# Kernel tuning notes

Hardware: AMD Instinct MI355X
Metric: run time of the kernel (lower is better)

## Reference

```python
import jax, jax.numpy as jnp
import numpy as np

DIM = 1024
NUM_HEADS = 16
HEAD_DIM = DIM // NUM_HEADS
ROPE_BASE = 10000.0


def _rope_cache(seq_len, head_dim, dtype=jnp.float32):
    inv_freq = 1.0 / (ROPE_BASE ** (jnp.arange(0, head_dim, 2, dtype=jnp.float32) / head_dim))
    t = jnp.arange(seq_len, dtype=jnp.float32)
    freqs = jnp.einsum('i,j->ij', t, inv_freq)          # [S, hd/2]
    emb = jnp.concatenate([freqs, freqs], axis=-1)       # [S, hd]
    return jnp.cos(emb).astype(dtype), jnp.sin(emb).astype(dtype)


def _rotate_half(x):
    x1, x2 = jnp.split(x, 2, axis=-1)
    return jnp.concatenate([-x2, x1], axis=-1)


def setup_inputs() -> dict:
    key = jax.random.key(0)
    k1, k2, k3 = jax.random.split(key, 3)
    B, S, D = 2, 2048, DIM
    x = jax.random.normal(k1, (B, S, D), dtype=jnp.float32)
    mask = jnp.tril(jnp.ones((S, S), dtype=jnp.bool_))   # causal mask
    w_qkv = jax.random.normal(k2, (D, 3 * D), dtype=jnp.float32) * (D ** -0.5)
    w_out = jax.random.normal(k3, (D, D), dtype=jnp.float32) * (D ** -0.5)
    return {"x": x, "w_qkv": w_qkv, "w_out": w_out, "mask": mask}


def reference(x, w_qkv, w_out, mask):
    B, S, D = x.shape
    H, hd = NUM_HEADS, HEAD_DIM
    qkv = x @ w_qkv                                       # [B,S,3D]
    q, k, v = jnp.split(qkv, 3, axis=-1)
    # [B,H,S,hd]
    q = q.reshape(B, S, H, hd).transpose(0, 2, 1, 3)
    k = k.reshape(B, S, H, hd).transpose(0, 2, 1, 3)
    v = v.reshape(B, S, H, hd).transpose(0, 2, 1, 3)
    cos, sin = _rope_cache(S, hd, q.dtype)               # [S,hd]
    q = q * cos + _rotate_half(q) * sin
    k = k * cos + _rotate_half(k) * sin
    scale = hd ** -0.5
    scores = jnp.einsum('bhqd,bhkd->bhqk', q, k) * scale  # [B,H,S,S]
    neg = jnp.finfo(scores.dtype).min
    scores = jnp.where(mask[None, None, :, :], scores, neg)
    attn = jax.nn.softmax(scores, axis=-1)                # dropout off (eval)
    out = jnp.einsum('bhqk,bhkd->bhqd', attn, v)
    out = out.transpose(0, 2, 1, 3).reshape(B, S, D)
    return out @ w_out
```

## Files before the change

### kernel.cpp

```cpp
#include <hip/hip_runtime.h>

typedef __attribute__((ext_vector_type(8))) short short8;
typedef __attribute__((ext_vector_type(4))) float f32x4;
typedef __attribute__((ext_vector_type(16))) float f32x16;

__device__ __forceinline__ unsigned short f2bf(float f) {
    unsigned u = __builtin_bit_cast(unsigned, f);
    u += 0x7FFFu + ((u >> 16) & 1u);
    return (unsigned short)(u >> 16);
}
__device__ __forceinline__ float bf2f(unsigned short b) {
    unsigned u = ((unsigned)b) << 16;
    return __builtin_bit_cast(float, u);
}
__device__ __forceinline__ short8 ld_frag(const uint4* p, size_t idx16) {
    return __builtin_bit_cast(short8, p[idx16]);
}
__device__ __forceinline__ unsigned cvt_pk_bf16(float lo, float hi) {
    unsigned r;
    asm("v_cvt_pk_bf16_f32 %0, %1, %2" : "=v"(r) : "v"(lo), "v"(hi));
    return r;
}
__device__ __forceinline__ void gload_lds16(const void* g, void* l) {
    __builtin_amdgcn_global_load_lds((const __attribute__((address_space(1))) void*)g,
                                     (__attribute__((address_space(3))) void*)l, 16, 0, 0);
}

__global__ void rope_table_kernel(float* cosT, float* sinT) {
    int idx = blockIdx.x * 256 + threadIdx.x;
    int s = idx >> 5, i = idx & 31;
    float inv = powf(10000.f, -(float)i / 32.f);
    float ang = (float)s * inv;
    cosT[idx] = cosf(ang);
    sinT[idx] = sinf(ang);
}

__global__ void cast_x_kernel(const float* __restrict__ x, unsigned short* __restrict__ xb) {
    int i = blockIdx.x * 256 + threadIdx.x;
    float4 v = reinterpret_cast<const float4*>(x)[i];
    ushort4 o;
    o.x = f2bf(v.x); o.y = f2bf(v.y); o.z = f2bf(v.z); o.w = f2bf(v.w);
    reinterpret_cast<ushort4*>(xb)[i] = o;
}

__global__ void transpose_cast_kernel(const float* __restrict__ in, unsigned short* __restrict__ out,
                                      int R, int C) {
    __shared__ float t[32][33];
    int c0 = blockIdx.x * 32, r0 = blockIdx.y * 32;
    int tx = threadIdx.x, ty = threadIdx.y;
    for (int i = 0; i < 4; ++i)
        t[ty + i * 8][tx] = in[(size_t)(r0 + ty + i * 8) * C + c0 + tx];
    __syncthreads();
    for (int i = 0; i < 4; ++i)
        out[(size_t)(c0 + ty + i * 8) * R + r0 + tx] = f2bf(t[tx][ty + i * 8]);
}

template <bool OUT_BF16, int NF>
__global__ __launch_bounds__(256) void gemm_bt_kernel(const unsigned short* __restrict__ A,
                                                      const unsigned short* __restrict__ Bt,
                                                      void* __restrict__ Cout,
                                                      int M, int N, int K) {
    constexpr int BN = NF * 32;
    __shared__ __align__(16) unsigned short As[2][128 * 32];
    __shared__ __align__(16) unsigned short Bs[2][BN * 32];
    int tid = threadIdx.x;
    int lane = tid & 63;
    int w = tid >> 6;
    int wm = w >> 1, wn = w & 1;
    int m0 = blockIdx.y * 128, n0 = blockIdx.x * BN;
    int rq = lane >> 4, cl = lane & 15;

    f32x4 acc[4][NF] = {};
    const uint4* As4 = reinterpret_cast<const uint4*>(As);
    const uint4* Bs4 = reinterpret_cast<const uint4*>(Bs);

    #pragma unroll
    for (int i = 0; i < 2; ++i) {
        int c = i * 256 + tid;
        int r = c >> 2, cc = c & 3;
        gload_lds16(A + (size_t)(m0 + r) * K + cc * 8,
                    (char*)As[0] + (size_t)(i * 256 + w * 64) * 16);
    }
    #pragma unroll
    for (int i = 0; i < NF / 2; ++i) {
        int c = i * 256 + tid;
        int r = c >> 2, cc = c & 3;
        gload_lds16(Bt + (size_t)(n0 + r) * K + cc * 8,
                    (char*)Bs[0] + (size_t)(i * 256 + w * 64) * 16);
    }
    __syncthreads();
    int cur = 0;

    for (int k0 = 0; k0 < K; k0 += 32) {
        short8 af[4], bfr[NF];
        #pragma unroll
        for (int mf = 0; mf < 4; ++mf) {
            int row = wm * 64 + mf * 16 + cl;
            af[mf] = ld_frag(As4, cur * 512 + row * 4 + rq);
        }
        #pragma unroll
        for (int nf = 0; nf < NF; ++nf) {
            int row = wn * (NF * 16) + nf * 16 + cl;
            bfr[nf] = ld_frag(Bs4, cur * (NF * 128) + row * 4 + rq);
        }
        if (k0 + 32 < K) {
            int kn = k0 + 32;
            #pragma unroll
            for (int i = 0; i < 2; ++i) {
                int c = i * 256 + tid;
                int r = c >> 2, cc = c & 3;
                gload_lds16(A + (size_t)(m0 + r) * K + kn + cc * 8,
                            (char*)As[cur ^ 1] + (size_t)(i * 256 + w * 64) * 16);
            }
            #pragma unroll
            for (int i = 0; i < NF / 2; ++i) {
                int c = i * 256 + tid;
                int r = c >> 2, cc = c & 3;
                gload_lds16(Bt + (size_t)(n0 + r) * K + kn + cc * 8,
                            (char*)Bs[cur ^ 1] + (size_t)(i * 256 + w * 64) * 16);
            }
        }
        __builtin_amdgcn_s_setprio(1);
        #pragma unroll
        for (int mf = 0; mf < 4; ++mf)
            #pragma unroll
            for (int nf = 0; nf < NF; ++nf)
                acc[mf][nf] = __builtin_amdgcn_mfma_f32_16x16x32_bf16(af[mf], bfr[nf], acc[mf][nf], 0, 0, 0);
        __builtin_amdgcn_s_setprio(0);
        __syncthreads();
        cur ^= 1;
    }
    #pragma unroll
    for (int mf = 0; mf < 4; ++mf)
        #pragma unroll
        for (int nf = 0; nf < NF; ++nf)
            #pragma unroll
            for (int r = 0; r < 4; ++r) {
                size_t row = m0 + wm * 64 + mf * 16 + rq * 4 + r;
                size_t col = n0 + wn * (NF * 16) + nf * 16 + cl;
                float v = acc[mf][nf][r];
                if (OUT_BF16)
                    ((unsigned short*)Cout)[row * N + col] = f2bf(v);
                else
                    ((float*)Cout)[row * N + col] = v;
            }
}

__global__ __launch_bounds__(256) void gemm_qkv_rope_kernel(const unsigned short* __restrict__ A,
                                                            const unsigned short* __restrict__ Bt,
                                                            const float* __restrict__ cosT,
                                                            const float* __restrict__ sinT,
                                                            unsigned short* __restrict__ Qb,
                                                            unsigned short* __restrict__ Kb,
                                                            unsigned short* __restrict__ VT) {
    const int K = 1024;
    __shared__ __align__(16) unsigned short As[2][128 * 32];
    __shared__ __align__(16) unsigned short Bs[2][128 * 32];
    int tid = threadIdx.x;
    int lane = tid & 63;
    int w = tid >> 6;
    int wm = w >> 1, wn = w & 1;
    int m0 = blockIdx.y * 128, n0 = blockIdx.x * 128;
    int rq = lane >> 4, cl = lane & 15;

    f32x4 acc[4][4] = {};
    const uint4* As4 = reinterpret_cast<const uint4*>(As);
    const uint4* Bs4 = reinterpret_cast<const uint4*>(Bs);

    #pragma unroll
    for (int i = 0; i < 2; ++i) {
        int c = i * 256 + tid;
        int r = c >> 2, cc = c & 3;
        gload_lds16(A + (size_t)(m0 + r) * K + cc * 8,
                    (char*)As[0] + (size_t)(i * 256 + w * 64) * 16);
        gload_lds16(Bt + (size_t)(n0 + r) * K + cc * 8,
                    (char*)Bs[0] + (size_t)(i * 256 + w * 64) * 16);
    }
    __syncthreads();
    int cur = 0;

    for (int k0 = 0; k0 < K; k0 += 32) {
        short8 af[4], bfr[4];
        #pragma unroll
        for (int mf = 0; mf < 4; ++mf)
            af[mf] = ld_frag(As4, cur * 512 + (wm * 64 + mf * 16 + cl) * 4 + rq);
        #pragma unroll
        for (int nf = 0; nf < 4; ++nf)
            bfr[nf] = ld_frag(Bs4, cur * 512 + (wn * 64 + nf * 16 + cl) * 4 + rq);
        if (k0 + 32 < K) {
            int kn = k0 + 32;
            #pragma unroll
            for (int i = 0; i < 2; ++i) {
                int c = i * 256 + tid;
                int r = c >> 2, cc = c & 3;
                gload_lds16(A + (size_t)(m0 + r) * K + kn + cc * 8,
                            (char*)As[cur ^ 1] + (size_t)(i * 256 + w * 64) * 16);
                gload_lds16(Bt + (size_t)(n0 + r) * K + kn + cc * 8,
                            (char*)Bs[cur ^ 1] + (size_t)(i * 256 + w * 64) * 16);
            }
        }
        __builtin_amdgcn_s_setprio(1);
        #pragma unroll
        for (int mf = 0; mf < 4; ++mf)
            #pragma unroll
            for (int nf = 0; nf < 4; ++nf)
                acc[mf][nf] = __builtin_amdgcn_mfma_f32_16x16x32_bf16(af[mf], bfr[nf], acc[mf][nf], 0, 0, 0);
        __builtin_amdgcn_s_setprio(0);
        __syncthreads();
        cur ^= 1;
    }

    const float QSCALE = 0.125f * 1.44269504088896f;
    int colbase = n0 + wn * 64;
    int sect = colbase >> 10;
    int h = (colbase >> 6) & 15;
    #pragma unroll
    for (int mf = 0; mf < 4; ++mf) {
        int row0 = m0 + wm * 64 + mf * 16 + rq * 4;
        int b = row0 >> 11;
        int s0r = row0 & 2047;
        size_t ho = (size_t)(b * 16 + h);
        if (sect == 2) {
            #pragma unroll
            for (int nf = 0; nf < 4; ++nf) {
                int d = nf * 16 + cl;
                ushort4 o;
                o.x = f2bf(acc[mf][nf][0]);
                o.y = f2bf(acc[mf][nf][1]);
                o.z = f2bf(acc[mf][nf][2]);
                o.w = f2bf(acc[mf][nf][3]);
                *reinterpret_cast<ushort4*>(VT + (ho * 64 + d) * 2048 + s0r) = o;
            }
        } else {
            unsigned short* dst = (sect == 0) ? Qb : Kb;
            float scale = (sect == 0) ? QSCALE : 1.0f;
            #pragma unroll
            for (int nf = 0; nf < 4; ++nf) {
                int d = nf * 16 + cl;
                int f = ((nf & 1) << 4) + cl;
                #pragma unroll
                for (int r = 0; r < 4; ++r) {
                    int s = s0r + r;
                    float cs = cosT[s * 32 + f], sn = sinT[s * 32 + f];
                    float val = acc[mf][nf][r], pair = acc[mf][nf ^ 2][r];
                    float out = (nf < 2) ? val * cs - pair * sn : val * cs + pair * sn;
                    dst[(ho * 2048 + s) * 64 + d] = f2bf(out * scale);
                }
            }
        }
    }
}

__global__ __launch_bounds__(256) void flash_attn_kernel(const unsigned short* __restrict__ Qb,
                                                         const unsigned short* __restrict__ Kb,
                                                         const unsigned short* __restrict__ VT,
                                                         unsigned short* __restrict__ Oattn) {
    const int S = 2048;
    __shared__ __align__(16) char smem[4 * 8192 + 512];
    char* KsB = smem;
    char* VsB = smem + 2 * 8192;
    int tid = threadIdx.x, lane = tid & 63, w = tid >> 6;
    int qsub = w & 1, kvh = w >> 1;
    int gid = blockIdx.x;
    int hh = gid & 31;
    int cp = gid >> 5;
    size_t headOff = (size_t)hh * S * 64;
    const unsigned short* Kg = Kb + headOff;
    const unsigned short* Vg = VT + headOff;
    const uint4* Qg4 = reinterpret_cast<const uint4*>(Qb + headOff);
    int l31 = lane & 31, hi = lane >> 5;

    int sr[2], sj[2];
    #pragma unroll
    for (int i = 0; i < 2; ++i) {
        int cch = i * 256 + tid;
        sr[i] = cch >> 3;
        sj[i] = ((cch & 7) ^ (sr[i] & 7)) * 8;
    }
    float* mo = reinterpret_cast<float*>(smem);
    float* ml = reinterpret_cast<float*>(smem + 16384);

    #pragma unroll
    for (int ph = 0; ph < 2; ++ph) {
        int c = ph ? (31 - cp) : cp;
        int q0 = c * 64;
        int qw = q0 + qsub * 32;
        int qrow = qw + l31;

        short8 qf[4];
        #pragma unroll
        for (int cc = 0; cc < 4; ++cc)
            qf[cc] = ld_frag(Qg4, (size_t)qrow * 8 + cc * 2 + hi);

        f32x16 oacc0 = {}, oacc1 = {};
        float l = 0.f;
        int nk = c + 1;

        #pragma unroll
        for (int i = 0; i < 2; ++i) {
            gload_lds16(Kg + sr[i] * 64 + sj[i], KsB + (i * 256 + w * 64) * 16);
            gload_lds16(Vg + (size_t)sr[i] * S + sj[i], VsB + (i * 256 + w * 64) * 16);
        }
        __syncthreads();
        int cur = 0;

        for (int kt = 0; kt < nk; ++kt) {
            int kv0 = kt * 64;
            int kvbase = kv0 + kvh * 32;
            bool active = kvbase <= qw + 31;
            short8 ka[4], va[4];
            if (active) {
                const char* Kt = KsB + cur * 8192;
                const char* Vt = VsB + cur * 8192;
                int r = kvh * 32 + l31;
                #pragma unroll
                for (int cc = 0; cc < 4; ++cc)
                    ka[cc] = __builtin_bit_cast(short8, *reinterpret_cast<const uint4*>(
                        Kt + r * 128 + (((2 * cc + hi) ^ (r & 7)) * 16)));
                #pragma unroll
                for (int t = 0; t < 2; ++t) {
                    va[t] = __builtin_bit_cast(short8, *reinterpret_cast<const uint4*>(
                        Vt + l31 * 128 + (((kvh * 4 + 2 * t + hi) ^ (l31 & 7)) * 16)));
                    va[2 + t] = __builtin_bit_cast(short8, *reinterpret_cast<const uint4*>(
                        Vt + (32 + l31) * 128 + (((kvh * 4 + 2 * t + hi) ^ ((32 + l31) & 7)) * 16)));
                }
            }
            if (kt + 1 < nk) {
                int kn = kv0 + 64;
                #pragma unroll
                for (int i = 0; i < 2; ++i) {
                    gload_lds16(Kg + (kn + sr[i]) * 64 + sj[i],
                                KsB + (cur ^ 1) * 8192 + (i * 256 + w * 64) * 16);
                    gload_lds16(Vg + (size_t)sr[i] * S + kn + sj[i],
                                VsB + (cur ^ 1) * 8192 + (i * 256 + w * 64) * 16);
                }
            }
            if (active) {
                f32x16 s = {};
                __builtin_amdgcn_s_setprio(1);
                #pragma unroll
                for (int cc = 0; cc < 4; ++cc)
                    s = __builtin_amdgcn_mfma_f32_32x32x16_bf16(ka[cc], qf[cc], s, 0, 0, 0);
                __builtin_amdgcn_s_setprio(0);

                if (kvbase + 31 > qw) {
                    #pragma unroll
                    for (int r = 0; r < 16; ++r) {
                        int kva = kvbase + (r & 3) + 8 * (r >> 2) + 4 * hi;
                        s[r] = (kva <= qrow) ? s[r] : -1e30f;
                    }
                }
                #pragma unroll
                for (int r = 0; r < 16; ++r) s[r] = exp2f(s[r]);
                float rp0 = ((s[0] + s[4]) + (s[8] + s[12])) + ((s[1] + s[5]) + (s[9] + s[13]));
                float rp1 = ((s[2] + s[6]) + (s[10] + s[14])) + ((s[3] + s[7]) + (s[11] + s[15]));
                float rs = rp0 + rp1;
                rs += __shfl_xor(rs, 32);
                l += rs;

                unsigned wd[8];
                #pragma unroll
                for (int i = 0; i < 8; ++i) wd[i] = cvt_pk_bf16(s[2 * i], s[2 * i + 1]);
                unsigned e0 = (unsigned)__shfl_xor((int)(hi ? wd[0] : wd[2]), 32);
                unsigned e1 = (unsigned)__shfl_xor((int)(hi ? wd[1] : wd[3]), 32);
                unsigned e2 = (unsigned)__shfl_xor((int)(hi ? wd[4] : wd[6]), 32);
                unsigned e3 = (unsigned)__shfl_xor((int)(hi ? wd[5] : wd[7]), 32);
                uint4 p0 = hi ? uint4{e0, e1, wd[2], wd[3]} : uint4{wd[0], wd[1], e0, e1};
                uint4 p1 = hi ? uint4{e2, e3, wd[6], wd[7]} : uint4{wd[4], wd[5], e2, e3};
                short8 pb0 = __builtin_bit_cast(short8, p0);
                short8 pb1 = __builtin_bit_cast(short8, p1);

                __builtin_amdgcn_s_setprio(1);
                oacc0 = __builtin_amdgcn_mfma_f32_32x32x16_bf16(va[0], pb0, oacc0, 0, 0, 0);
                oacc0 = __builtin_amdgcn_mfma_f32_32x32x16_bf16(va[1], pb1, oacc0, 0, 0, 0);
                oacc1 = __builtin_amdgcn_mfma_f32_32x32x16_bf16(va[2], pb0, oacc1, 0, 0, 0);
                oacc1 = __builtin_amdgcn_mfma_f32_32x32x16_bf16(va[3], pb1, oacc1, 0, 0, 0);
                __builtin_amdgcn_s_setprio(0);
            }
            __syncthreads();
            cur ^= 1;
        }

        if (kvh) {
            #pragma unroll
            for (int r = 0; r < 16; ++r) {
                mo[(r * 2 + qsub) * 64 + lane]        = oacc0[r];
                mo[((16 + r) * 2 + qsub) * 64 + lane] = oacc1[r];
            }
            ml[qsub * 64 + lane] = l;
        }
        __syncthreads();
        if (!kvh) {
            l += ml[qsub * 64 + lane];
            float invl = 1.f / l;
            size_t orow = ((size_t)((hh >> 4) * 2048 + qrow)) * 1024 + (hh & 15) * 64;
            #pragma unroll
            for (int du = 0; du < 2; ++du) {
                const f32x16& oa = du ? oacc1 : oacc0;
                #pragma unroll
                for (int gq = 0; gq < 4; ++gq) {
                    ushort4 o;
                    #pragma unroll
                    for (int e = 0; e < 4; ++e) {
                        int r = 4 * gq + e;
                        float v = (oa[r] + mo[((du * 16 + r) * 2 + qsub) * 64 + lane]) * invl;
                        ((unsigned short*)&o)[e] = f2bf(v);
                    }
                    int d = du * 32 + 4 * hi + 8 * gq;
                    *reinterpret_cast<ushort4*>(Oattn + orow + d) = o;
                }
            }
        }
        __syncthreads();
    }
}

extern "C" void kernel_launch(void* const* d_in, const int* in_sizes, int n_in,
                              void* d_out, int out_size, void* d_ws, size_t ws_size,
                              hipStream_t stream) {
    const float* x    = (const float*)d_in[0];
    const float* wqkv = (const float*)d_in[1];
    const float* wout = (const float*)d_in[2];

    char* ws = (char*)d_ws;
    unsigned short* xb    = (unsigned short*)(ws);
    unsigned short* wqkvT = (unsigned short*)(ws + (8ull  << 20));
    unsigned short* woutT = (unsigned short*)(ws + (14ull << 20));
    unsigned short* Qb    = (unsigned short*)(ws + (40ull << 20));
    unsigned short* Kb    = (unsigned short*)(ws + (48ull << 20));
    unsigned short* VT    = (unsigned short*)(ws + (56ull << 20));
    unsigned short* Oat   = (unsigned short*)(ws + (64ull << 20));
    float* cosT           = (float*)(ws + (72ull << 20));
    float* sinT           = (float*)(ws + (72ull << 20) + (256u << 10));

    rope_table_kernel<<<256, 256, 0, stream>>>(cosT, sinT);
    cast_x_kernel<<<4096, 256, 0, stream>>>(x, xb);
    transpose_cast_kernel<<<dim3(96, 32), dim3(32, 8), 0, stream>>>(wqkv, wqkvT, 1024, 3072);
    transpose_cast_kernel<<<dim3(32, 32), dim3(32, 8), 0, stream>>>(wout, woutT, 1024, 1024);
    gemm_qkv_rope_kernel<<<dim3(24, 32), 256, 0, stream>>>(xb, wqkvT, cosT, sinT, Qb, Kb, VT);
    flash_attn_kernel<<<512, 256, 0, stream>>>(Qb, Kb, VT, Oat);
    gemm_bt_kernel<false, 2><<<dim3(16, 32), 256, 0, stream>>>(Oat, woutT, d_out, 4096, 1024, 1024);
}
```

Baseline: 120.6 us.

## Split KV tiles across two wave groups in flash attention and fuse prep kernels

Flash attention blocks grow to 512 threads, with two wave groups processing alternate KV tiles in parallel from separate double-buffered LDS regions. Partial outputs from four wave groups are reduced through shared memory at the end. The four preprocessing kernels (rope table, x cast, two weight transposes) are merged into one launch to cut launch overhead. The larger LDS footprint and block size may reduce occupancy, and the final reduction adds shared-memory traffic.

```diff
diff --git a/kernel.cpp b/kernel.cpp
--- a/kernel.cpp
+++ b/kernel.cpp
@@ -9,10 +9,6 @@
     u += 0x7FFFu + ((u >> 16) & 1u);
     return (unsigned short)(u >> 16);
 }
-__device__ __forceinline__ float bf2f(unsigned short b) {
-    unsigned u = ((unsigned)b) << 16;
-    return __builtin_bit_cast(float, u);
-}
 __device__ __forceinline__ short8 ld_frag(const uint4* p, size_t idx16) {
     return __builtin_bit_cast(short8, p[idx16]);
 }
@@ -26,28 +22,40 @@
                                      (__attribute__((address_space(3))) void*)l, 16, 0, 0);
 }
 
-__global__ void rope_table_kernel(float* cosT, float* sinT) {
-    int idx = blockIdx.x * 256 + threadIdx.x;
-    int s = idx >> 5, i = idx & 31;
-    float inv = powf(10000.f, -(float)i / 32.f);
-    float ang = (float)s * inv;
-    cosT[idx] = cosf(ang);
-    sinT[idx] = sinf(ang);
-}
-
-__global__ void cast_x_kernel(const float* __restrict__ x, unsigned short* __restrict__ xb) {
-    int i = blockIdx.x * 256 + threadIdx.x;
-    float4 v = reinterpret_cast<const float4*>(x)[i];
-    ushort4 o;
-    o.x = f2bf(v.x); o.y = f2bf(v.y); o.z = f2bf(v.z); o.w = f2bf(v.w);
-    reinterpret_cast<ushort4*>(xb)[i] = o;
-}
-
-__global__ void transpose_cast_kernel(const float* __restrict__ in, unsigned short* __restrict__ out,
-                                      int R, int C) {
+__global__ __launch_bounds__(256) void prep_kernel(const float* __restrict__ x, unsigned short* __restrict__ xb,
+                                                   const float* __restrict__ wqkv, unsigned short* __restrict__ wqkvT,
+                                                   const float* __restrict__ wout, unsigned short* __restrict__ woutT,
+                                                   float* __restrict__ cosT, float* __restrict__ sinT) {
     __shared__ float t[32][33];
-    int c0 = blockIdx.x * 32, r0 = blockIdx.y * 32;
-    int tx = threadIdx.x, ty = threadIdx.y;
+    int bid = blockIdx.x, tid = threadIdx.x;
+    if (bid < 256) {
+        int idx = bid * 256 + tid;
+        int s = idx >> 5, i = idx & 31;
+        float inv = powf(10000.f, -(float)i / 32.f);
+        float ang = (float)s * inv;
+        cosT[idx] = cosf(ang);
+        sinT[idx] = sinf(ang);
+        return;
+    }
+    if (bid < 4352) {
+        int i = (bid - 256) * 256 + tid;
+        float4 v = reinterpret_cast<const float4*>(x)[i];
+        ushort4 o;
+        o.x = f2bf(v.x); o.y = f2bf(v.y); o.z = f2bf(v.z); o.w = f2bf(v.w);
+        reinterpret_cast<ushort4*>(xb)[i] = o;
+        return;
+    }
+    const float* in; unsigned short* out; int R, C, c0, r0;
+    if (bid < 7424) {
+        int b2 = bid - 4352;
+        in = wqkv; out = wqkvT; R = 1024; C = 3072;
+        c0 = (b2 % 96) * 32; r0 = (b2 / 96) * 32;
+    } else {
+        int b2 = bid - 7424;
+        in = wout; out = woutT; R = 1024; C = 1024;
+        c0 = (b2 % 32) * 32; r0 = (b2 / 32) * 32;
+    }
+    int tx = tid & 31, ty = tid >> 5;
     for (int i = 0; i < 4; ++i)
         t[ty + i * 8][tx] = in[(size_t)(r0 + ty + i * 8) * C + c0 + tx];
     __syncthreads();
@@ -251,16 +259,14 @@
     }
 }
 
-__global__ __launch_bounds__(256) void flash_attn_kernel(const unsigned short* __restrict__ Qb,
+__global__ __launch_bounds__(512) void flash_attn_kernel(const unsigned short* __restrict__ Qb,
                                                          const unsigned short* __restrict__ Kb,
                                                          const unsigned short* __restrict__ VT,
                                                          unsigned short* __restrict__ Oattn) {
     const int S = 2048;
-    __shared__ __align__(16) char smem[4 * 8192 + 512];
-    char* KsB = smem;
-    char* VsB = smem + 2 * 8192;
+    __shared__ __align__(16) char smem[65536 + 512];
     int tid = threadIdx.x, lane = tid & 63, w = tid >> 6;
-    int qsub = w & 1, kvh = w >> 1;
+    int qsub = w & 1, kvh = (w >> 1) & 1, st = w >> 2;
     int gid = blockIdx.x;
     int hh = gid & 31;
     int cp = gid >> 5;
@@ -270,15 +276,12 @@
     const uint4* Qg4 = reinterpret_cast<const uint4*>(Qb + headOff);
     int l31 = lane & 31, hi = lane >> 5;
 
-    int sr[2], sj[2];
-    #pragma unroll
-    for (int i = 0; i < 2; ++i) {
-        int cch = i * 256 + tid;
-        sr[i] = cch >> 3;
-        sj[i] = ((cch & 7) ^ (sr[i] & 7)) * 8;
-    }
+    int sr = tid >> 3;
+    int sj = ((tid & 7) ^ (sr & 7)) * 8;
+    char* Kst = smem + st * 16384;
+    char* Vst = smem + 32768 + st * 16384;
     float* mo = reinterpret_cast<float*>(smem);
-    float* ml = reinterpret_cast<float*>(smem + 16384);
+    float* ml = reinterpret_cast<float*>(smem + 49152);
 
     #pragma unroll
     for (int ph = 0; ph < 2; ++ph) {
@@ -286,6 +289,8 @@
         int q0 = c * 64;
         int qw = q0 + qsub * 32;
         int qrow = qw + l31;
+        int nk = c + 1;
+        int nr = (nk + 1) >> 1;
 
         short8 qf[4];
         #pragma unroll
@@ -294,24 +299,24 @@
 
         f32x16 oacc0 = {}, oacc1 = {};
         float l = 0.f;
-        int nk = c + 1;
-
-        #pragma unroll
-        for (int i = 0; i < 2; ++i) {
-            gload_lds16(Kg + sr[i] * 64 + sj[i], KsB + (i * 256 + w * 64) * 16);
-            gload_lds16(Vg + (size_t)sr[i] * S + sj[i], VsB + (i * 256 + w * 64) * 16);
+
+        gload_lds16(Kg + (0 * 64 + sr) * 64 + sj, smem + 0 * 16384 + tid * 16);
+        gload_lds16(Vg + (size_t)sr * S + 0 * 64 + sj, smem + 32768 + 0 * 16384 + tid * 16);
+        if (nk > 1) {
+            gload_lds16(Kg + (1 * 64 + sr) * 64 + sj, smem + 1 * 16384 + tid * 16);
+            gload_lds16(Vg + (size_t)sr * S + 1 * 64 + sj, smem + 32768 + 1 * 16384 + tid * 16);
         }
         __syncthreads();
         int cur = 0;
 
-        for (int kt = 0; kt < nk; ++kt) {
-            int kv0 = kt * 64;
-            int kvbase = kv0 + kvh * 32;
-            bool active = kvbase <= qw + 31;
+        for (int rd = 0; rd < nr; ++rd) {
+            int kt = 2 * rd + st;
+            int kvbase = kt * 64 + kvh * 32;
+            bool active = (kt < nk) && (kvbase <= qw + 31);
             short8 ka[4], va[4];
             if (active) {
-                const char* Kt = KsB + cur * 8192;
-                const char* Vt = VsB + cur * 8192;
+                const char* Kt = Kst + cur * 8192;
+                const char* Vt = Vst + cur * 8192;
                 int r = kvh * 32 + l31;
                 #pragma unroll
                 for (int cc = 0; cc < 4; ++cc)
@@ -325,14 +330,19 @@
                         Vt + (32 + l31) * 128 + (((kvh * 4 + 2 * t + hi) ^ ((32 + l31) & 7)) * 16)));
                 }
             }
-            if (kt + 1 < nk) {
-                int kn = kv0 + 64;
-                #pragma unroll
-                for (int i = 0; i < 2; ++i) {
-                    gload_lds16(Kg + (kn + sr[i]) * 64 + sj[i],
-                                KsB + (cur ^ 1) * 8192 + (i * 256 + w * 64) * 16);
-                    gload_lds16(Vg + (size_t)sr[i] * S + kn + sj[i],
-                                VsB + (cur ^ 1) * 8192 + (i * 256 + w * 64) * 16);
+            {
+                int kt2 = 2 * rd + 2;
+                if (kt2 < nk) {
+                    gload_lds16(Kg + (kt2 * 64 + sr) * 64 + sj,
+                                smem + 0 * 16384 + (cur ^ 1) * 8192 + tid * 16);
+                    gload_lds16(Vg + (size_t)sr * S + kt2 * 64 + sj,
+                                smem + 32768 + 0 * 16384 + (cur ^ 1) * 8192 + tid * 16);
+                }
+                if (kt2 + 1 < nk) {
+                    gload_lds16(Kg + ((kt2 + 1) * 64 + sr) * 64 + sj,
+                                smem + 1 * 16384 + (cur ^ 1) * 8192 + tid * 16);
+                    gload_lds16(Vg + (size_t)sr * S + (kt2 + 1) * 64 + sj,
+                                smem + 32768 + 1 * 16384 + (cur ^ 1) * 8192 + tid * 16);
                 }
             }
             if (active) {
@@ -381,17 +391,26 @@
             cur ^= 1;
         }
 
-        if (kvh) {
+        int pub = (kvh << 1 | st) - 1;
+        if (pub >= 0) {
             #pragma unroll
             for (int r = 0; r < 16; ++r) {
-                mo[(r * 2 + qsub) * 64 + lane]        = oacc0[r];
-                mo[((16 + r) * 2 + qsub) * 64 + lane] = oacc1[r];
-            }
-            ml[qsub * 64 + lane] = l;
+                mo[((pub * 32 + r) * 2 + qsub) * 64 + lane]      = oacc0[r];
+                mo[((pub * 32 + 16 + r) * 2 + qsub) * 64 + lane] = oacc1[r];
+            }
+            ml[(pub * 2 + qsub) * 64 + lane] = l;
         }
         __syncthreads();
-        if (!kvh) {
-            l += ml[qsub * 64 + lane];
+        if (pub < 0) {
+            #pragma unroll
+            for (int p = 0; p < 3; ++p) {
+                l += ml[(p * 2 + qsub) * 64 + lane];
+                #pragma unroll
+                for (int r = 0; r < 16; ++r) {
+                    oacc0[r] += mo[((p * 32 + r) * 2 + qsub) * 64 + lane];
+                    oacc1[r] += mo[((p * 32 + 16 + r) * 2 + qsub) * 64 + lane];
+                }
+            }
             float invl = 1.f / l;
             size_t orow = ((size_t)((hh >> 4) * 2048 + qrow)) * 1024 + (hh & 15) * 64;
             #pragma unroll
@@ -401,11 +420,8 @@
                 for (int gq = 0; gq < 4; ++gq) {
                     ushort4 o;
                     #pragma unroll
-                    for (int e = 0; e < 4; ++e) {
-                        int r = 4 * gq + e;
-                        float v = (oa[r] + mo[((du * 16 + r) * 2 + qsub) * 64 + lane]) * invl;
-                        ((unsigned short*)&o)[e] = f2bf(v);
-                    }
+                    for (int e = 0; e < 4; ++e)
+                        ((unsigned short*)&o)[e] = f2bf(oa[4 * gq + e] * invl);
                     int d = du * 32 + 4 * hi + 8 * gq;
                     *reinterpret_cast<ushort4*>(Oattn + orow + d) = o;
                 }
@@ -433,11 +449,8 @@
     float* cosT           = (float*)(ws + (72ull << 20));
     float* sinT           = (float*)(ws + (72ull << 20) + (256u << 10));
 
-    rope_table_kernel<<<256, 256, 0, stream>>>(cosT, sinT);
-    cast_x_kernel<<<4096, 256, 0, stream>>>(x, xb);
-    transpose_cast_kernel<<<dim3(96, 32), dim3(32, 8), 0, stream>>>(wqkv, wqkvT, 1024, 3072);
-    transpose_cast_kernel<<<dim3(32, 32), dim3(32, 8), 0, stream>>>(wout, woutT, 1024, 1024);
+    prep_kernel<<<8448, 256, 0, stream>>>(x, xb, wqkv, wqkvT, wout, woutT, cosT, sinT);
     gemm_qkv_rope_kernel<<<dim3(24, 32), 256, 0, stream>>>(xb, wqkvT, cosT, sinT, Qb, Kb, VT);
-    flash_attn_kernel<<<512, 256, 0, stream>>>(Qb, Kb, VT, Oat);
+    flash_attn_kernel<<<512, 512, 0, stream>>>(Qb, Kb, VT, Oat);
     gemm_bt_kernel<false, 2><<<dim3(16, 32), 256, 0, stream>>>(Oat, woutT, d_out, 4096, 1024, 1024);
 }
```

Result: faster. 115.3 us (-4.4%).

## Fuse x fp32-to-bf16 cast into QKV GEMM and merge prep kernels

Applied to the files above, without the earlier changes.

Removes the separate cast_x kernel: the QKV GEMM now streams fp32 x tiles into LDS with an XOR swizzle and converts them to bf16 in registers before the MFMAs. The rope table and both weight transpose-casts are merged into one prep launch. This removes the bf16 x intermediate round-trip and three kernel launches. In exchange, the GEMM reads twice as many A bytes from global memory and uses double the LDS for A, with extra conversion instructions in the inner loop.

```diff
diff --git a/kernel.cpp b/kernel.cpp
--- a/kernel.cpp
+++ b/kernel.cpp
@@ -9,10 +9,6 @@
     u += 0x7FFFu + ((u >> 16) & 1u);
     return (unsigned short)(u >> 16);
 }
-__device__ __forceinline__ float bf2f(unsigned short b) {
-    unsigned u = ((unsigned)b) << 16;
-    return __builtin_bit_cast(float, u);
-}
 __device__ __forceinline__ short8 ld_frag(const uint4* p, size_t idx16) {
     return __builtin_bit_cast(short8, p[idx16]);
 }
@@ -26,28 +22,31 @@
                                      (__attribute__((address_space(3))) void*)l, 16, 0, 0);
 }
 
-__global__ void rope_table_kernel(float* cosT, float* sinT) {
-    int idx = blockIdx.x * 256 + threadIdx.x;
-    int s = idx >> 5, i = idx & 31;
-    float inv = powf(10000.f, -(float)i / 32.f);
-    float ang = (float)s * inv;
-    cosT[idx] = cosf(ang);
-    sinT[idx] = sinf(ang);
-}
-
-__global__ void cast_x_kernel(const float* __restrict__ x, unsigned short* __restrict__ xb) {
-    int i = blockIdx.x * 256 + threadIdx.x;
-    float4 v = reinterpret_cast<const float4*>(x)[i];
-    ushort4 o;
-    o.x = f2bf(v.x); o.y = f2bf(v.y); o.z = f2bf(v.z); o.w = f2bf(v.w);
-    reinterpret_cast<ushort4*>(xb)[i] = o;
-}
-
-__global__ void transpose_cast_kernel(const float* __restrict__ in, unsigned short* __restrict__ out,
-                                      int R, int C) {
+__global__ __launch_bounds__(256) void prep_kernel(const float* __restrict__ wqkv, unsigned short* __restrict__ wqkvT,
+                                                   const float* __restrict__ wout, unsigned short* __restrict__ woutT,
+                                                   float* __restrict__ cosT, float* __restrict__ sinT) {
     __shared__ float t[32][33];
-    int c0 = blockIdx.x * 32, r0 = blockIdx.y * 32;
-    int tx = threadIdx.x, ty = threadIdx.y;
+    int bid = blockIdx.x, tid = threadIdx.x;
+    if (bid < 256) {
+        int idx = bid * 256 + tid;
+        int s = idx >> 5, i = idx & 31;
+        float inv = powf(10000.f, -(float)i / 32.f);
+        float ang = (float)s * inv;
+        cosT[idx] = cosf(ang);
+        sinT[idx] = sinf(ang);
+        return;
+    }
+    const float* in; unsigned short* out; int R, C, c0, r0;
+    if (bid < 3328) {
+        int b2 = bid - 256;
+        in = wqkv; out = wqkvT; R = 1024; C = 3072;
+        c0 = (b2 % 96) * 32; r0 = (b2 / 96) * 32;
+    } else {
+        int b2 = bid - 3328;
+        in = wout; out = woutT; R = 1024; C = 1024;
+        c0 = (b2 % 32) * 32; r0 = (b2 / 32) * 32;
+    }
+    int tx = tid & 31, ty = tid >> 5;
     for (int i = 0; i < 4; ++i)
         t[ty + i * 8][tx] = in[(size_t)(r0 + ty + i * 8) * C + c0 + tx];
     __syncthreads();
@@ -146,7 +145,7 @@
             }
 }
 
-__global__ __launch_bounds__(256) void gemm_qkv_rope_kernel(const unsigned short* __restrict__ A,
+__global__ __launch_bounds__(256) void gemm_qkv_rope_kernel(const float* __restrict__ A,
                                                             const unsigned short* __restrict__ Bt,
                                                             const float* __restrict__ cosT,
                                                             const float* __restrict__ sinT,
@@ -154,7 +153,7 @@
                                                             unsigned short* __restrict__ Kb,
                                                             unsigned short* __restrict__ VT) {
     const int K = 1024;
-    __shared__ __align__(16) unsigned short As[2][128 * 32];
+    __shared__ __align__(16) float Asf[2][128 * 32];
     __shared__ __align__(16) unsigned short Bs[2][128 * 32];
     int tid = threadIdx.x;
     int lane = tid & 63;
@@ -164,40 +163,56 @@
     int rq = lane >> 4, cl = lane & 15;
 
     f32x4 acc[4][4] = {};
-    const uint4* As4 = reinterpret_cast<const uint4*>(As);
+    const uint4* As4 = reinterpret_cast<const uint4*>(Asf);
     const uint4* Bs4 = reinterpret_cast<const uint4*>(Bs);
 
-    #pragma unroll
-    for (int i = 0; i < 2; ++i) {
-        int c = i * 256 + tid;
-        int r = c >> 2, cc = c & 3;
-        gload_lds16(A + (size_t)(m0 + r) * K + cc * 8,
-                    (char*)As[0] + (size_t)(i * 256 + w * 64) * 16);
-        gload_lds16(Bt + (size_t)(n0 + r) * K + cc * 8,
-                    (char*)Bs[0] + (size_t)(i * 256 + w * 64) * 16);
-    }
+    auto stageA = [&](int k0, int buf) {
+        #pragma unroll
+        for (int i = 0; i < 4; ++i) {
+            int c = i * 256 + tid;
+            int r = c >> 3, c8 = c & 7;
+            gload_lds16(A + (size_t)(m0 + r) * K + k0 + ((c8 ^ (r & 7)) * 4),
+                        (char*)Asf[buf] + (size_t)(i * 256 + w * 64) * 16);
+        }
+    };
+    auto stageB = [&](int k0, int buf) {
+        #pragma unroll
+        for (int i = 0; i < 2; ++i) {
+            int c = i * 256 + tid;
+            int r = c >> 2, cc = c & 3;
+            gload_lds16(Bt + (size_t)(n0 + r) * K + k0 + cc * 8,
+                        (char*)Bs[buf] + (size_t)(i * 256 + w * 64) * 16);
+        }
+    };
+
+    stageA(0, 0);
+    stageB(0, 0);
     __syncthreads();
     int cur = 0;
 
     for (int k0 = 0; k0 < K; k0 += 32) {
         short8 af[4], bfr[4];
         #pragma unroll
-        for (int mf = 0; mf < 4; ++mf)
-            af[mf] = ld_frag(As4, cur * 512 + (wm * 64 + mf * 16 + cl) * 4 + rq);
+        for (int mf = 0; mf < 4; ++mf) {
+            int row = wm * 64 + mf * 16 + cl;
+            int p0 = (rq * 2) ^ (row & 7);
+            uint4 x0 = As4[cur * 1024 + row * 8 + p0];
+            uint4 x1 = As4[cur * 1024 + row * 8 + (p0 ^ 1)];
+            f32x4 f0 = __builtin_bit_cast(f32x4, x0);
+            f32x4 f1 = __builtin_bit_cast(f32x4, x1);
+            unsigned pk[4];
+            pk[0] = cvt_pk_bf16(f0[0], f0[1]);
+            pk[1] = cvt_pk_bf16(f0[2], f0[3]);
+            pk[2] = cvt_pk_bf16(f1[0], f1[1]);
+            pk[3] = cvt_pk_bf16(f1[2], f1[3]);
+            af[mf] = __builtin_bit_cast(short8, uint4{pk[0], pk[1], pk[2], pk[3]});
+        }
         #pragma unroll
         for (int nf = 0; nf < 4; ++nf)
             bfr[nf] = ld_frag(Bs4, cur * 512 + (wn * 64 + nf * 16 + cl) * 4 + rq);
         if (k0 + 32 < K) {
-            int kn = k0 + 32;
-            #pragma unroll
-            for (int i = 0; i < 2; ++i) {
-                int c = i * 256 + tid;
-                int r = c >> 2, cc = c & 3;
-                gload_lds16(A + (size_t)(m0 + r) * K + kn + cc * 8,
-                            (char*)As[cur ^ 1] + (size_t)(i * 256 + w * 64) * 16);
-                gload_lds16(Bt + (size_t)(n0 + r) * K + kn + cc * 8,
-                            (char*)Bs[cur ^ 1] + (size_t)(i * 256 + w * 64) * 16);
-            }
+            stageA(k0 + 32, cur ^ 1);
+            stageB(k0 + 32, cur ^ 1);
         }
         __builtin_amdgcn_s_setprio(1);
         #pragma unroll
@@ -423,7 +438,6 @@
     const float* wout = (const float*)d_in[2];
 
     char* ws = (char*)d_ws;
-    unsigned short* xb    = (unsigned short*)(ws);
     unsigned short* wqkvT = (unsigned short*)(ws + (8ull  << 20));
     unsigned short* woutT = (unsigned short*)(ws + (14ull << 20));
     unsigned short* Qb    = (unsigned short*)(ws + (40ull << 20));
@@ -433,11 +447,8 @@
     float* cosT           = (float*)(ws + (72ull << 20));
     float* sinT           = (float*)(ws + (72ull << 20) + (256u << 10));
 
-    rope_table_kernel<<<256, 256, 0, stream>>>(cosT, sinT);
-    cast_x_kernel<<<4096, 256, 0, stream>>>(x, xb);
-    transpose_cast_kernel<<<dim3(96, 32), dim3(32, 8), 0, stream>>>(wqkv, wqkvT, 1024, 3072);
-    transpose_cast_kernel<<<dim3(32, 32), dim3(32, 8), 0, stream>>>(wout, woutT, 1024, 1024);
-    gemm_qkv_rope_kernel<<<dim3(24, 32), 256, 0, stream>>>(xb, wqkvT, cosT, sinT, Qb, Kb, VT);
+    prep_kernel<<<4352, 256, 0, stream>>>(wqkv, wqkvT, wout, woutT, cosT, sinT);
+    gemm_qkv_rope_kernel<<<dim3(24, 32), 256, 0, stream>>>(x, wqkvT, cosT, sinT, Qb, Kb, VT);
     flash_attn_kernel<<<512, 256, 0, stream>>>(Qb, Kb, VT, Oat);
     gemm_bt_kernel<false, 2><<<dim3(16, 32), 256, 0, stream>>>(Oat, woutT, d_out, 4096, 1024, 1024);
 }
```

New measurement: 131.5 us. 9.0% more time.
